# Optimization experiments

Measured on AMD Instinct MI355X. Metric: run time of the kernel, lower is better.

The kernel has to match this reference:

```python
import jax, jax.numpy as jnp
import numpy as np

BS, T, NE, NA, ED = 32, 64, 32, 8, 128
H, A, NH, NACT = 512, 512, 8, 32
HD = A // NH  # 64
SCALE = np.float32(np.sqrt(HD))


def setup_inputs() -> dict:
    key = jax.random.key(0)
    ks = jax.random.split(key, 12)
    inputs = jax.random.normal(ks[0], (BS, T, NE, ED), jnp.float32)
    obs_mask = jax.random.randint(ks[1], (BS, T, NE, NE), 0, 2, jnp.int32)
    scenario_mask = jax.random.randint(ks[2], (BS, T, NE), 0, 2, jnp.int32)
    hidden_state = jnp.zeros((BS * NA, H), jnp.float32)
    g = lambda k, shp: jax.random.normal(k, shp, jnp.float32) * 0.05
    return {
        'inputs': inputs, 'obs_mask': obs_mask, 'scenario_mask': scenario_mask,
        'hidden_state': hidden_state,
        'W1': g(ks[3], (ED, H)), 'b1': jnp.zeros((H,), jnp.float32),
        'Wq': g(ks[4], (H, A)), 'bq': jnp.zeros((A,), jnp.float32),
        'Wk': g(ks[5], (H, A)), 'bk': jnp.zeros((A,), jnp.float32),
        'Wv': g(ks[6], (H, A)), 'bv': jnp.zeros((A,), jnp.float32),
        'Wih': g(ks[7], (3 * H, A)), 'bih': jnp.zeros((3 * H,), jnp.float32),
        'Whh': g(ks[8], (3 * H, H)), 'bhh': jnp.zeros((3 * H,), jnp.float32),
        'Wo': g(ks[9], (H, NACT)), 'bo': jnp.zeros((NACT,), jnp.float32),
    }


def reference(inputs, obs_mask, scenario_mask, hidden_state,
              W1, b1, Wq, bq, Wk, bk, Wv, bv, Wih, bih, Whh, bhh, Wo, bo):
    # fc1: embed every entity  [BS,T,NE,H]
    x = jax.nn.relu(inputs @ W1 + b1)
    q = (x @ Wq + bq).reshape(BS, T, NE, NH, HD)[:, :, :NA]   # agent queries
    k = (x @ Wk + bk).reshape(BS, T, NE, NH, HD)
    v = jax.nn.relu(x @ Wv + bv).reshape(BS, T, NE, NH, HD)
    # scores [BS,T,NH,NA,NE]
    score = jnp.einsum('btqhe,btkhe->bthqk', q, k) / SCALE
    am = obs_mask[:, :, :NA, :].astype(bool)                  # [BS,T,NA,NE]
    score = jnp.where(am[:, :, None], -jnp.inf, score)
    w = jax.nn.softmax(score, axis=-1)
    w = jnp.where(jnp.isnan(w), 0.0, w)                       # fully-masked rows -> 0
    att = jnp.einsum('bthqk,btkhe->btqhe', w, v).reshape(BS, T, NA, A)
    agent_mask = scenario_mask[:, :, :NA].astype(bool)        # [BS,T,NA]
    att = jnp.where(agent_mask[..., None], 0.0, att)
    # per-timestep GRUCell over flattened (BS*NA) rows
    xs = att.transpose(1, 0, 2, 3).reshape(T, BS * NA, A)
    def step(h, xt):
        gi = xt @ Wih.T + bih
        gh = h @ Whh.T + bhh
        ir, iz, inn = jnp.split(gi, 3, axis=-1)
        hr, hz, hn = jnp.split(gh, 3, axis=-1)
        r = jax.nn.sigmoid(ir + hr)
        z = jax.nn.sigmoid(iz + hz)
        n = jnp.tanh(inn + r * hn)
        hn_ = (1.0 - z) * n + z * h
        return hn_, hn_
    _, hs = jax.lax.scan(step, hidden_state, xs)              # [T,BS*NA,H]
    hs = hs.reshape(T, BS, NA, H).transpose(1, 0, 2, 3)       # [BS,T,NA,H]
    qout = hs @ Wo + bo                                       # [BS,T,NA,NACT]
    hs = jnp.where(agent_mask[..., None], 0.0, hs)
    qout = jnp.where(agent_mask[..., None], 0.0, qout)
    return qout, hs
```

## Files before the change

### kernel.cpp

```cpp
#include <hip/hip_runtime.h>
#include <hip/hip_bf16.h>
#include <cstddef>
#include <cstdint>

typedef __hip_bfloat16 bf16;
typedef __attribute__((ext_vector_type(2))) _Float16 half2v;
typedef __attribute__((ext_vector_type(8))) _Float16 half8;
typedef __attribute__((ext_vector_type(8))) short short8;
typedef __attribute__((ext_vector_type(4))) float f32x4;
typedef __attribute__((ext_vector_type(2))) unsigned long long u64x2;

__device__ inline float ldf(const float* p) { return *p; }
__device__ inline float ldf(const bf16* p) { return __bfloat162float(*p); }
__device__ inline void stf(float* p, float v) { *p = v; }
__device__ inline void stf(bf16* p, float v) { *p = __float2bfloat16(v); }
__device__ inline short bfb(float v) { return __builtin_bit_cast(short, __float2bfloat16(v)); }

__device__ inline half8 h8_from(unsigned long long lo, unsigned long long hi) {
    u64x2 t; t.x = lo; t.y = hi;
    return __builtin_bit_cast(half8, t);
}
__device__ inline float fsig(float x) {
    x = fminf(fmaxf(x, -60.f), 60.f);
    return 1.f / (1.f + __expf(-x));
}
__device__ inline float ftanh(float x) {
    x = fminf(fmaxf(x, -15.f), 15.f);
    float e = __expf(2.f * x);
    return 1.f - 2.f / (e + 1.f);
}
__device__ inline void unpack8(uint4 u, float4& lo, float4& hi) {
    uint32_t w0 = u.x, w1 = u.y, w2 = u.z, w3 = u.w;
    lo.x = __builtin_bit_cast(float, (w0 & 0xffffu) << 16);
    lo.y = __builtin_bit_cast(float, w0 & 0xffff0000u);
    lo.z = __builtin_bit_cast(float, (w1 & 0xffffu) << 16);
    lo.w = __builtin_bit_cast(float, w1 & 0xffff0000u);
    hi.x = __builtin_bit_cast(float, (w2 & 0xffffu) << 16);
    hi.y = __builtin_bit_cast(float, w2 & 0xffff0000u);
    hi.z = __builtin_bit_cast(float, (w3 & 0xffffu) << 16);
    hi.w = __builtin_bit_cast(float, w3 & 0xffff0000u);
}


template<int ACT, bool QG, typename TA, typename TC>
__global__ __launch_bounds__(256) void mfma_gemm_k(
    const TA* __restrict__ A, const bf16* __restrict__ Bt,
    const float* __restrict__ bias, TC* __restrict__ C,
    int M, int N, int K)
{
    __shared__ short As[4096];
    __shared__ short Bs[4096];
    const int tid = threadIdx.x;
    const int lane = tid & 63, wid = tid >> 6;
    const int wm = wid >> 1, wn = wid & 1;
    const int bm = blockIdx.y * 128, bn = blockIdx.x * 128;
    const int fr = lane & 15, fq = lane >> 4;

    f32x4 acc[4][4] = {};

    for (int k0 = 0; k0 < K; k0 += 32) {
#if __has_builtin(__builtin_amdgcn_global_load_lds)
        #pragma unroll
        for (int j = 0; j < 2; ++j) {
            int jj = wid * 2 + j;
            int row = jj * 16 + (lane >> 2);
            const short* src = (const short*)Bt + (size_t)(bn + row) * K + k0 + (lane & 3) * 8;
            __builtin_amdgcn_global_load_lds(
                (const __attribute__((address_space(1))) void*)src,
                (__attribute__((address_space(3))) void*)&Bs[jj * 512], 16, 0, 0);
        }
        if constexpr (sizeof(TA) == 2) {
            #pragma unroll
            for (int j = 0; j < 2; ++j) {
                int jj = wid * 2 + j;
                int row = jj * 16 + (lane >> 2);
                int gm = bm + row;
                int ar = QG ? (((gm >> 3) << 5) | (gm & 7)) : gm;
                const short* src = (const short*)A + (size_t)ar * K + k0 + (lane & 3) * 8;
                __builtin_amdgcn_global_load_lds(
                    (const __attribute__((address_space(1))) void*)src,
                    (__attribute__((address_space(3))) void*)&As[jj * 512], 16, 0, 0);
            }
        } else {
            int sr = tid >> 1, sk = (tid & 1) * 16;
            int gm = bm + sr;
            int ar = QG ? (((gm >> 3) << 5) | (gm & 7)) : gm;
            const float* ap = (const float*)A + (size_t)ar * K + k0 + sk;
            float4 f0 = *(const float4*)(ap);
            float4 f1 = *(const float4*)(ap + 4);
            float4 f2 = *(const float4*)(ap + 8);
            float4 f3 = *(const float4*)(ap + 12);
            short tmp[16] = {bfb(f0.x), bfb(f0.y), bfb(f0.z), bfb(f0.w),
                             bfb(f1.x), bfb(f1.y), bfb(f1.z), bfb(f1.w),
                             bfb(f2.x), bfb(f2.y), bfb(f2.z), bfb(f2.w),
                             bfb(f3.x), bfb(f3.y), bfb(f3.z), bfb(f3.w)};
            *(uint4*)&As[sr * 32 + sk]     = *(const uint4*)&tmp[0];
            *(uint4*)&As[sr * 32 + sk + 8] = *(const uint4*)&tmp[8];
        }
#else
        {
            int sr = tid >> 1, sk = (tid & 1) * 16;
            int gm = bm + sr;
            int ar = QG ? (((gm >> 3) << 5) | (gm & 7)) : gm;
            if constexpr (sizeof(TA) == 4) {
                const float* ap = (const float*)A + (size_t)ar * K + k0 + sk;
                short tmp[16];
                #pragma unroll
                for (int j = 0; j < 16; ++j) tmp[j] = bfb(ap[j]);
                *(uint4*)&As[sr * 32 + sk]     = *(const uint4*)&tmp[0];
                *(uint4*)&As[sr * 32 + sk + 8] = *(const uint4*)&tmp[8];
            } else {
                const short* ap = (const short*)A + (size_t)ar * K + k0 + sk;
                *(uint4*)&As[sr * 32 + sk]     = *(const uint4*)(ap);
                *(uint4*)&As[sr * 32 + sk + 8] = *(const uint4*)(ap + 8);
            }
            const short* bp = (const short*)Bt + (size_t)(bn + sr) * K + k0 + sk;
            *(uint4*)&Bs[sr * 32 + sk]     = *(const uint4*)(bp);
            *(uint4*)&Bs[sr * 32 + sk + 8] = *(const uint4*)(bp + 8);
        }
#endif
        __syncthreads();

        short8 af[4], bg[4];
        #pragma unroll
        for (int m = 0; m < 4; ++m)
            af[m] = *(const short8*)&As[(wm * 64 + m * 16 + fr) * 32 + fq * 8];
        #pragma unroll
        for (int n = 0; n < 4; ++n)
            bg[n] = *(const short8*)&Bs[(wn * 64 + n * 16 + fr) * 32 + fq * 8];
        #pragma unroll
        for (int m = 0; m < 4; ++m)
            #pragma unroll
            for (int n = 0; n < 4; ++n)
                acc[m][n] = __builtin_amdgcn_mfma_f32_16x16x32_bf16(
                    af[m], bg[n], acc[m][n], 0, 0, 0);
        __syncthreads();
    }

    #pragma unroll
    for (int m = 0; m < 4; ++m) {
        #pragma unroll
        for (int n = 0; n < 4; ++n) {
            int col = bn + wn * 64 + n * 16 + fr;
            float bv = bias[col];
            #pragma unroll
            for (int r = 0; r < 4; ++r) {
                int row = bm + wm * 64 + m * 16 + fq * 4 + r;
                float v = acc[m][n][r] + bv;
                if (ACT == 1) v = fmaxf(v, 0.f);
                if (ACT == 2 && col >= 512) v = fmaxf(v, 0.f);
                stf(&C[(size_t)row * N + col], v);
            }
        }
    }
}

__global__ __launch_bounds__(256) void prep_all_k(
    const float* __restrict__ W1, const float* __restrict__ Wq,
    const float* __restrict__ Wk, const float* __restrict__ Wv,
    const float* __restrict__ Wo, const float* __restrict__ h0,
    const float* __restrict__ bk, const float* __restrict__ bv,
    bf16* __restrict__ W1t, bf16* __restrict__ Wqt, bf16* __restrict__ Wkvt,
    bf16* __restrict__ Wot, _Float16* __restrict__ ha, float* __restrict__ bkv)
{
    int blk = blockIdx.x;
    int tid = threadIdx.x;
    if (blk < 848) {
        const float* src; bf16* dst; int K, N, ti;
        if (blk < 64)       { src = W1; dst = W1t;  K = 128; N = 512; ti = blk; }
        else if (blk < 320) { src = Wq; dst = Wqt;  K = 512; N = 512; ti = blk - 64; }
        else if (blk < 576) { src = Wk; dst = Wkvt; K = 512; N = 512; ti = blk - 320; }
        else if (blk < 832) { src = Wv; dst = Wkvt + 512 * 512; K = 512; N = 512; ti = blk - 576; }
        else                { src = Wo; dst = Wot;  K = 512; N = 32;  ti = blk - 832; }
        int kt = K >> 5;
        int tk = ti % kt, tn = ti / kt;
        int k0 = tk * 32, n0 = tn * 32;
        __shared__ float tile[32][33];
        int tx = tid & 31, ty = tid >> 5;
        #pragma unroll
        for (int i = 0; i < 4; ++i) {
            int r = ty + i * 8;
            tile[r][tx] = src[(size_t)(k0 + r) * N + n0 + tx];
        }
        __syncthreads();
        #pragma unroll
        for (int i = 0; i < 4; ++i) {
            int r = ty + i * 8;
            if (n0 + r < N)
                dst[(size_t)(n0 + r) * K + k0 + tx] = __float2bfloat16(tile[tx][r]);
        }
        return;
    }
    int idx = (blk - 848) * 256 + tid;
    if (idx < 131072) { ha[idx] = (_Float16)h0[idx]; return; }
    idx -= 131072;
    if (idx < 1024) { bkv[idx] = (idx < 512) ? bk[idx] : bv[idx - 512]; return; }
}

__global__ __launch_bounds__(256) void qout_mfma_k(
    const float* __restrict__ hs, const bf16* __restrict__ Wot,
    const float* __restrict__ bo, const int* __restrict__ smask,
    float* __restrict__ out)
{
    __shared__ short Bs2[32 * 520];
    __shared__ short As2[128 * 32];
    const int tid = threadIdx.x;
    const int lane = tid & 63, wid = tid >> 6;
    const int bm = blockIdx.x * 128;
    const int fr = lane & 15, fq = lane >> 4;

    for (int i = tid; i < 2048; i += 256) {
        int row = i >> 6, col = (i & 63) * 8;
        *(uint4*)&Bs2[row * 520 + col] = *(const uint4*)((const short*)Wot + row * 512 + col);
    }

    f32x4 acc[2][2] = {};
    for (int k0 = 0; k0 < 512; k0 += 32) {
        {
            int sr = tid >> 1, sk = (tid & 1) * 16;
            const float* ap = hs + (size_t)(bm + sr) * 512 + k0 + sk;
            float4 f0 = *(const float4*)(ap);
            float4 f1 = *(const float4*)(ap + 4);
            float4 f2 = *(const float4*)(ap + 8);
            float4 f3 = *(const float4*)(ap + 12);
            short tmp[16] = {bfb(f0.x), bfb(f0.y), bfb(f0.z), bfb(f0.w),
                             bfb(f1.x), bfb(f1.y), bfb(f1.z), bfb(f1.w),
                             bfb(f2.x), bfb(f2.y), bfb(f2.z), bfb(f2.w),
                             bfb(f3.x), bfb(f3.y), bfb(f3.z), bfb(f3.w)};
            *(uint4*)&As2[sr * 32 + sk]     = *(const uint4*)&tmp[0];
            *(uint4*)&As2[sr * 32 + sk + 8] = *(const uint4*)&tmp[8];
        }
        __syncthreads();
        short8 af[2], bg[2];
        #pragma unroll
        for (int m = 0; m < 2; ++m)
            af[m] = *(const short8*)&As2[(wid * 32 + m * 16 + fr) * 32 + fq * 8];
        #pragma unroll
        for (int n = 0; n < 2; ++n)
            bg[n] = *(const short8*)&Bs2[(n * 16 + fr) * 520 + k0 + fq * 8];
        #pragma unroll
        for (int m = 0; m < 2; ++m)
            #pragma unroll
            for (int n = 0; n < 2; ++n)
                acc[m][n] = __builtin_amdgcn_mfma_f32_16x16x32_bf16(
                    af[m], bg[n], acc[m][n], 0, 0, 0);
        __syncthreads();
    }

    #pragma unroll
    for (int m = 0; m < 2; ++m) {
        #pragma unroll
        for (int n = 0; n < 2; ++n) {
            int col = n * 16 + fr;
            float bv = bo[col];
            #pragma unroll
            for (int r = 0; r < 4; ++r) {
                int row = bm + wid * 32 + m * 16 + fq * 4 + r;
                int a_ = row & 7, t_ = (row >> 3) & 63, b_ = row >> 9;
                bool mz = smask[((b_ << 6) + t_) * 32 + a_] != 0;
                out[(size_t)row * 32 + col] = mz ? 0.f : (acc[m][n][r] + bv);
            }
        }
    }
}

#define AST 68
__global__ __launch_bounds__(64) void attn_k(
    const bf16* __restrict__ qb, const bf16* __restrict__ kb, const bf16* __restrict__ vb,
    const int* __restrict__ obs, const int* __restrict__ smask, bf16* __restrict__ xs,
    int kvstride)
{
    __shared__ float qs[8 * AST], ks[32 * AST], vs[32 * AST], wsm[8 * 32];
    int bid = blockIdx.x;
    int h = bid & 7;
    int bt = bid >> 3;
    int t = bt & 63, b = bt >> 6;
    int tid = threadIdx.x;

    {
        int srow = tid >> 3, c0 = (tid & 7) * 8;
        float4 lo, hi;
        uint4 qv = *(const uint4*)&qb[((size_t)bt * 8 + srow) * 512 + h * 64 + c0];
        unpack8(qv, lo, hi);
        *(float4*)&qs[srow * AST + c0] = lo;
        *(float4*)&qs[srow * AST + c0 + 4] = hi;
        #pragma unroll
        for (int i = 0; i < 4; ++i) {
            int row = srow + i * 8;
            uint4 kv4 = *(const uint4*)&kb[((size_t)bt * 32 + row) * kvstride + h * 64 + c0];
            unpack8(kv4, lo, hi);
            *(float4*)&ks[row * AST + c0] = lo;
            *(float4*)&ks[row * AST + c0 + 4] = hi;
            uint4 vv4 = *(const uint4*)&vb[((size_t)bt * 32 + row) * kvstride + h * 64 + c0];
            unpack8(vv4, lo, hi);
            *(float4*)&vs[row * AST + c0] = lo;
            *(float4*)&vs[row * AST + c0 + 4] = hi;
        }
    }
    __syncthreads();

    int ql = tid >> 3, jl = tid & 7;
    float s[4];
    #pragma unroll
    for (int c = 0; c < 4; ++c) {
        int kl = jl + c * 8;
        float acc = 0.f;
        for (int d = 0; d < 64; ++d) acc += qs[ql * AST + d] * ks[kl * AST + d];
        acc *= 0.125f;
        bool m = obs[(((size_t)bt * 32) + ql) * 32 + kl] != 0;
        s[c] = m ? -__builtin_inff() : acc;
    }
    float mx = fmaxf(fmaxf(s[0], s[1]), fmaxf(s[2], s[3]));
    for (int off = 1; off < 8; off <<= 1) mx = fmaxf(mx, __shfl_xor(mx, off));
    float e4[4]; float sum = 0.f;
    bool allmasked = (mx == -__builtin_inff());
    #pragma unroll
    for (int c = 0; c < 4; ++c) {
        e4[c] = (allmasked || s[c] == -__builtin_inff()) ? 0.f : expf(s[c] - mx);
        sum += e4[c];
    }
    for (int off = 1; off < 8; off <<= 1) sum += __shfl_xor(sum, off);
    float inv = (sum > 0.f) ? 1.f / sum : 0.f;
    #pragma unroll
    for (int c = 0; c < 4; ++c) wsm[ql * 32 + jl + c * 8] = e4[c] * inv;
    __syncthreads();

    bool amask = smask[(size_t)bt * 32 + ql] != 0;
    #pragma unroll
    for (int dd = 0; dd < 8; ++dd) {
        int d = jl + dd * 8;
        float acc = 0.f;
        for (int kl = 0; kl < 32; ++kl) acc += wsm[ql * 32 + kl] * vs[kl * AST + d];
        if (amask) acc = 0.f;
        xs[((size_t)(t * 256 + b * 8 + ql)) * 512 + h * 64 + d] = __float2bfloat16(acc);
    }
}

__global__ __launch_bounds__(128, 1) void gru_xcd_k(
    const bf16* __restrict__ xs, const float* __restrict__ Wih,
    const float* __restrict__ bih,
    const float* __restrict__ Whh, const float* __restrict__ bhh,
    const float* __restrict__ h0,
    const int* __restrict__ smask, float* __restrict__ hs_out,
    _Float16* __restrict__ ha, _Float16* __restrict__ hb,
    unsigned char* __restrict__ flags8)
{
    __shared__ _Float16 wh16[48 * 520];
    __shared__ short    wi16[48 * 520];
    const int tid = threadIdx.x;
    const int lane = tid & 63, wid = tid >> 6;
    const int g = blockIdx.x;
    const int grp = g & 7, cu = g >> 3;
    const int r0 = grp * 32;
    const int hc0 = cu * 16;
    const int fr = lane & 15, fq = lane >> 4;
    const int hcol = hc0 + fr;
    const int rw0 = r0 + wid * 16;
    const int row0 = rw0 + fq * 4;

    for (int i = tid; i < 6144; i += 128) {
        int flat = i * 4;
        int r = flat >> 9, c = flat & 511;
        int wr = (r >> 4) * 512 + hc0 + (r & 15);
        float4 v = *(const float4*)(Whh + (size_t)wr * 512 + c);
        half2v p0; p0[0] = (_Float16)v.x; p0[1] = (_Float16)v.y;
        half2v p1; p1[0] = (_Float16)v.z; p1[1] = (_Float16)v.w;
        *(uint32_t*)&wh16[r * 520 + c]     = __builtin_bit_cast(uint32_t, p0);
        *(uint32_t*)&wh16[r * 520 + c + 2] = __builtin_bit_cast(uint32_t, p1);
        float4 u = *(const float4*)(Wih + (size_t)wr * 512 + c);
        uint32_t w0 = (uint32_t)(uint16_t)bfb(u.x) | ((uint32_t)(uint16_t)bfb(u.y) << 16);
        uint32_t w1 = (uint32_t)(uint16_t)bfb(u.z) | ((uint32_t)(uint16_t)bfb(u.w) << 16);
        *(uint32_t*)&wi16[r * 520 + c]     = w0;
        *(uint32_t*)&wi16[r * 520 + c + 2] = w1;
    }

    const float bhr = bhh[hcol], bhz = bhh[512 + hcol], bhn = bhh[1024 + hcol];
    const float bir = bih[hcol], biz = bih[512 + hcol], bin_ = bih[1024 + hcol];

    float hp[4];
    #pragma unroll
    for (int r = 0; r < 4; ++r)
        hp[r] = h0[(size_t)(row0 + r) * 512 + hcol];

    __syncthreads();

    f32x4 gcur[3] = {};
    int mcur[4];
    {
        const short* xp = (const short*)xs + ((size_t)0 * 256 + rw0 + fr) * 512 + fq * 8;
        short8 ax[16];
        #pragma unroll
        for (int ks = 0; ks < 16; ++ks) ax[ks] = *(const short8*)(xp + ks * 32);
        #pragma unroll
        for (int ks = 0; ks < 16; ++ks) {
            const short* bb = &wi16[fr * 520 + ks * 32 + fq * 8];
            short8 b0 = *(const short8*)(bb);
            short8 b1 = *(const short8*)(bb + 16 * 520);
            short8 b2 = *(const short8*)(bb + 32 * 520);
            gcur[0] = __builtin_amdgcn_mfma_f32_16x16x32_bf16(ax[ks], b0, gcur[0], 0, 0, 0);
            gcur[1] = __builtin_amdgcn_mfma_f32_16x16x32_bf16(ax[ks], b1, gcur[1], 0, 0, 0);
            gcur[2] = __builtin_amdgcn_mfma_f32_16x16x32_bf16(ax[ks], b2, gcur[2], 0, 0, 0);
        }
        #pragma unroll
        for (int r = 0; r < 4; ++r) {
            int row = row0 + r;
            mcur[r] = smask[(((row >> 3) << 6) + 0) * 32 + (row & 7)];
        }
    }

    for (int t = 0; t < 64; ++t) {
        const _Float16* hsrc = (t & 1) ? hb : ha;
        _Float16*       hdst = (t & 1) ? ha : hb;

        half8 aA[16];
        {
            const unsigned long long* ap = (const unsigned long long*)
                (hsrc + (size_t)(rw0 + fr) * 512 + fq * 8);
            #pragma unroll
            for (int ks = 0; ks < 16; ++ks) {
                unsigned long long lo = __hip_atomic_load(ap + ks * 8,
                    __ATOMIC_RELAXED, __HIP_MEMORY_SCOPE_AGENT);
                unsigned long long hi = __hip_atomic_load(ap + ks * 8 + 1,
                    __ATOMIC_RELAXED, __HIP_MEMORY_SCOPE_AGENT);
                aA[ks] = h8_from(lo, hi);
            }
        }

        f32x4 acc[3] = {};
        #pragma unroll
        for (int ks = 0; ks < 16; ++ks) {
            const _Float16* bbase = &wh16[fr * 520 + ks * 32 + fq * 8];
            half8 b0 = *(const half8*)(bbase);
            half8 b1 = *(const half8*)(bbase + 16 * 520);
            half8 b2 = *(const half8*)(bbase + 32 * 520);
            acc[0] = __builtin_amdgcn_mfma_f32_16x16x32_f16(aA[ks], b0, acc[0], 0, 0, 0);
            acc[1] = __builtin_amdgcn_mfma_f32_16x16x32_f16(aA[ks], b1, acc[1], 0, 0, 0);
            acc[2] = __builtin_amdgcn_mfma_f32_16x16x32_f16(aA[ks], b2, acc[2], 0, 0, 0);
        }

        float hnv[4];
        #pragma unroll
        for (int r = 0; r < 4; ++r) {
            float rg = fsig(gcur[0][r] + bir + acc[0][r] + bhr);
            float zg = fsig(gcur[1][r] + biz + acc[1][r] + bhz);
            float ng = ftanh(gcur[2][r] + bin_ + rg * (acc[2][r] + bhn));
            float hn = (1.f - zg) * ng + zg * hp[r];
            hp[r] = hn;
            hnv[r] = hn;
            unsigned short hbits = __builtin_bit_cast(unsigned short, (_Float16)hn);
            __hip_atomic_store((unsigned short*)(hdst + (size_t)(row0 + r) * 512 + hcol),
                               hbits, __ATOMIC_RELAXED, __HIP_MEMORY_SCOPE_AGENT);
        }

        if (t != 63) {
            asm volatile("s_waitcnt vmcnt(0)" ::: "memory");
            __builtin_amdgcn_sched_barrier(0);
            if (lane == 0)
                __hip_atomic_store(flags8 + ((size_t)grp * 64 + t) * 64 + cu * 2 + wid,
                                   (unsigned char)1,
                                   __ATOMIC_RELAXED, __HIP_MEMORY_SCOPE_AGENT);
            #pragma unroll
            for (int r = 0; r < 4; ++r) {
                int row = row0 + r;
                int b_ = row >> 3, a_ = row & 7;
                hs_out[((size_t)((b_ << 6) + t) * 8 + a_) * 512 + hcol] =
                    mcur[r] ? 0.f : hnv[r];
            }
            f32x4 gnx[3] = {};
            {
                const short* xp = (const short*)xs +
                    ((size_t)(t + 1) * 256 + rw0 + fr) * 512 + fq * 8;
                short8 ax[16];
                #pragma unroll
                for (int ks = 0; ks < 16; ++ks) ax[ks] = *(const short8*)(xp + ks * 32);
                #pragma unroll
                for (int ks = 0; ks < 16; ++ks) {
                    const short* bb = &wi16[fr * 520 + ks * 32 + fq * 8];
                    short8 b0 = *(const short8*)(bb);
                    short8 b1 = *(const short8*)(bb + 16 * 520);
                    short8 b2 = *(const short8*)(bb + 32 * 520);
                    gnx[0] = __builtin_amdgcn_mfma_f32_16x16x32_bf16(ax[ks], b0, gnx[0], 0, 0, 0);
                    gnx[1] = __builtin_amdgcn_mfma_f32_16x16x32_bf16(ax[ks], b1, gnx[1], 0, 0, 0);
                    gnx[2] = __builtin_amdgcn_mfma_f32_16x16x32_bf16(ax[ks], b2, gnx[2], 0, 0, 0);
                }
            }
            int mnx[4];
            #pragma unroll
            for (int r = 0; r < 4; ++r) {
                int row = row0 + r;
                mnx[r] = smask[(((row >> 3) << 6) + (t + 1)) * 32 + (row & 7)];
            }
            const unsigned char* fp = flags8 + ((size_t)grp * 64 + t) * 64 + lane;
            long it = 0;
            for (;;) {
                unsigned char f = __hip_atomic_load(fp, __ATOMIC_RELAXED,
                                                    __HIP_MEMORY_SCOPE_AGENT);
                if (__all(f != 0) || it > 200000000L) break;
                ++it;
            }
            __builtin_amdgcn_sched_barrier(0);
            gcur[0] = gnx[0]; gcur[1] = gnx[1]; gcur[2] = gnx[2];
            mcur[0] = mnx[0]; mcur[1] = mnx[1]; mcur[2] = mnx[2]; mcur[3] = mnx[3];
        } else {
            #pragma unroll
            for (int r = 0; r < 4; ++r) {
                int row = row0 + r;
                int b_ = row >> 3, a_ = row & 7;
                hs_out[((size_t)((b_ << 6) + t) * 8 + a_) * 512 + hcol] =
                    mcur[r] ? 0.f : hnv[r];
            }
        }
    }
}

extern "C" void kernel_launch(void* const* d_in, const int* in_sizes, int n_in,
                              void* d_out, int out_size, void* d_ws, size_t ws_size,
                              hipStream_t stream)
{
    const float* inputs = (const float*)d_in[0];
    const int*   obs    = (const int*)d_in[1];
    const int*   smask  = (const int*)d_in[2];
    const float* h0     = (const float*)d_in[3];
    const float* W1  = (const float*)d_in[4];  const float* b1  = (const float*)d_in[5];
    const float* Wq  = (const float*)d_in[6];  const float* bq  = (const float*)d_in[7];
    const float* Wk  = (const float*)d_in[8];  const float* bk  = (const float*)d_in[9];
    const float* Wv  = (const float*)d_in[10]; const float* bv  = (const float*)d_in[11];
    const float* Wih = (const float*)d_in[12]; const float* bih = (const float*)d_in[13];
    const float* Whh = (const float*)d_in[14]; const float* bhh = (const float*)d_in[15];
    const float* Wo  = (const float*)d_in[16]; const float* bo  = (const float*)d_in[17];

    char* ws = (char*)d_ws;
    bf16*  x    = (bf16*)(ws + 0);
    bf16*  xs   = (bf16*)(ws + 0);
    bf16*  qb   = (bf16*)(ws + 67108864ull);
    bf16*  kv   = (bf16*)(ws + 83886080ull);
    bf16*  W1t  = (bf16*)(ws + 218103808ull);
    bf16*  Wqt  = (bf16*)(ws + 218234880ull);
    bf16*  Wkvt = (bf16*)(ws + 218759168ull);
    _Float16* ha = (_Float16*)(ws + 219807744ull);
    _Float16* hb = (_Float16*)(ws + 220069888ull);
    unsigned char* flags8 = (unsigned char*)(ws + 220332032ull);
    float* bkv  = (float*)(ws + 220364800ull);
    bf16*  Wot  = (bf16*)(ws + 220368896ull);

    float* out    = (float*)d_out;
    float* hs_out = out + 524288;

    hipMemsetAsync(flags8, 0, 32768, stream);

    prep_all_k<<<dim3(1365), 256, 0, stream>>>(
        W1, Wq, Wk, Wv, Wo, h0, bk, bv, W1t, Wqt, Wkvt, Wot, ha, bkv);
    mfma_gemm_k<1, false, float, bf16><<<dim3(4, 512), 256, 0, stream>>>(
        inputs, W1t, b1, x, 65536, 512, 128);
    mfma_gemm_k<0, true, bf16, bf16><<<dim3(4, 128), 256, 0, stream>>>(
        x, Wqt, bq, qb, 16384, 512, 512);
    mfma_gemm_k<2, false, bf16, bf16><<<dim3(8, 512), 256, 0, stream>>>(
        x, Wkvt, bkv, kv, 65536, 1024, 512);
    attn_k<<<dim3(16384), 64, 0, stream>>>(qb, kv, kv + 512, obs, smask, xs, 1024);
    gru_xcd_k<<<dim3(256), 128, 0, stream>>>(
        xs, Wih, bih, Whh, bhh, h0, smask, hs_out, ha, hb, flags8);
    qout_mfma_k<<<dim3(128), 256, 0, stream>>>(hs_out, Wot, bo, smask, out);
}
```

Baseline: 642.6 us.

## Double-buffer GEMM LDS tiles and widen GRU sync flags with sleeping spin

The MFMA GEMM now keeps two LDS buffers for the A and B tiles. It issues the global-to-LDS loads for the next K-slice before computing on the current one, so load latency can overlap the MFMA work, at the cost of twice the shared memory per block. Separately, the GRU's inter-block step flags change from bytes to 32-bit ints, and the spin-wait loop gains an s_sleep. This is meant to cut memory contention from polling, but it may add wake-up latency on the sequential recurrence's critical path. The workspace offsets and the flag memset size are adjusted to match.

```diff
diff --git a/kernel.cpp b/kernel.cpp
--- a/kernel.cpp
+++ b/kernel.cpp
@@ -48,8 +48,8 @@
     const float* __restrict__ bias, TC* __restrict__ C,
     int M, int N, int K)
 {
-    __shared__ short As[4096];
-    __shared__ short Bs[4096];
+    __shared__ short As[2][4096];
+    __shared__ short Bs[2][4096];
     const int tid = threadIdx.x;
     const int lane = tid & 63, wid = tid >> 6;
     const int wm = wid >> 1, wn = wid & 1;
@@ -58,7 +58,7 @@
 
     f32x4 acc[4][4] = {};
 
-    for (int k0 = 0; k0 < K; k0 += 32) {
+    auto stage = [&](int buf, int k0) {
 #if __has_builtin(__builtin_amdgcn_global_load_lds)
         #pragma unroll
         for (int j = 0; j < 2; ++j) {
@@ -67,7 +67,7 @@
             const short* src = (const short*)Bt + (size_t)(bn + row) * K + k0 + (lane & 3) * 8;
             __builtin_amdgcn_global_load_lds(
                 (const __attribute__((address_space(1))) void*)src,
-                (__attribute__((address_space(3))) void*)&Bs[jj * 512], 16, 0, 0);
+                (__attribute__((address_space(3))) void*)&Bs[buf][jj * 512], 16, 0, 0);
         }
         if constexpr (sizeof(TA) == 2) {
             #pragma unroll
@@ -79,7 +79,7 @@
                 const short* src = (const short*)A + (size_t)ar * K + k0 + (lane & 3) * 8;
                 __builtin_amdgcn_global_load_lds(
                     (const __attribute__((address_space(1))) void*)src,
-                    (__attribute__((address_space(3))) void*)&As[jj * 512], 16, 0, 0);
+                    (__attribute__((address_space(3))) void*)&As[buf][jj * 512], 16, 0, 0);
             }
         } else {
             int sr = tid >> 1, sk = (tid & 1) * 16;
@@ -94,8 +94,8 @@
                              bfb(f1.x), bfb(f1.y), bfb(f1.z), bfb(f1.w),
                              bfb(f2.x), bfb(f2.y), bfb(f2.z), bfb(f2.w),
                              bfb(f3.x), bfb(f3.y), bfb(f3.z), bfb(f3.w)};
-            *(uint4*)&As[sr * 32 + sk]     = *(const uint4*)&tmp[0];
-            *(uint4*)&As[sr * 32 + sk + 8] = *(const uint4*)&tmp[8];
+            *(uint4*)&As[buf][sr * 32 + sk]     = *(const uint4*)&tmp[0];
+            *(uint4*)&As[buf][sr * 32 + sk + 8] = *(const uint4*)&tmp[8];
         }
 #else
         {
@@ -107,27 +107,35 @@
                 short tmp[16];
                 #pragma unroll
                 for (int j = 0; j < 16; ++j) tmp[j] = bfb(ap[j]);
-                *(uint4*)&As[sr * 32 + sk]     = *(const uint4*)&tmp[0];
-                *(uint4*)&As[sr * 32 + sk + 8] = *(const uint4*)&tmp[8];
+                *(uint4*)&As[buf][sr * 32 + sk]     = *(const uint4*)&tmp[0];
+                *(uint4*)&As[buf][sr * 32 + sk + 8] = *(const uint4*)&tmp[8];
             } else {
                 const short* ap = (const short*)A + (size_t)ar * K + k0 + sk;
-                *(uint4*)&As[sr * 32 + sk]     = *(const uint4*)(ap);
-                *(uint4*)&As[sr * 32 + sk + 8] = *(const uint4*)(ap + 8);
+                *(uint4*)&As[buf][sr * 32 + sk]     = *(const uint4*)(ap);
+                *(uint4*)&As[buf][sr * 32 + sk + 8] = *(const uint4*)(ap + 8);
             }
             const short* bp = (const short*)Bt + (size_t)(bn + sr) * K + k0 + sk;
-            *(uint4*)&Bs[sr * 32 + sk]     = *(const uint4*)(bp);
-            *(uint4*)&Bs[sr * 32 + sk + 8] = *(const uint4*)(bp + 8);
+            *(uint4*)&Bs[buf][sr * 32 + sk]     = *(const uint4*)(bp);
+            *(uint4*)&Bs[buf][sr * 32 + sk + 8] = *(const uint4*)(bp + 8);
         }
 #endif
-        __syncthreads();
+    };
+
+    const int nt = K >> 5;
+    stage(0, 0);
+    __syncthreads();
+
+    for (int t = 0; t < nt; ++t) {
+        int cur = t & 1;
+        if (t + 1 < nt) stage(cur ^ 1, (t + 1) * 32);
 
         short8 af[4], bg[4];
         #pragma unroll
         for (int m = 0; m < 4; ++m)
-            af[m] = *(const short8*)&As[(wm * 64 + m * 16 + fr) * 32 + fq * 8];
+            af[m] = *(const short8*)&As[cur][(wm * 64 + m * 16 + fr) * 32 + fq * 8];
         #pragma unroll
         for (int n = 0; n < 4; ++n)
-            bg[n] = *(const short8*)&Bs[(wn * 64 + n * 16 + fr) * 32 + fq * 8];
+            bg[n] = *(const short8*)&Bs[cur][(wn * 64 + n * 16 + fr) * 32 + fq * 8];
         #pragma unroll
         for (int m = 0; m < 4; ++m)
             #pragma unroll
@@ -342,8 +350,7 @@
     const float* __restrict__ Whh, const float* __restrict__ bhh,
     const float* __restrict__ h0,
     const int* __restrict__ smask, float* __restrict__ hs_out,
-    _Float16* __restrict__ ha, _Float16* __restrict__ hb,
-    unsigned char* __restrict__ flags8)
+    _Float16* __restrict__ ha, _Float16* __restrict__ hb, int* __restrict__ flags)
 {
     __shared__ _Float16 wh16[48 * 520];
     __shared__ short    wi16[48 * 520];
@@ -456,8 +463,7 @@
             asm volatile("s_waitcnt vmcnt(0)" ::: "memory");
             __builtin_amdgcn_sched_barrier(0);
             if (lane == 0)
-                __hip_atomic_store(flags8 + ((size_t)grp * 64 + t) * 64 + cu * 2 + wid,
-                                   (unsigned char)1,
+                __hip_atomic_store(flags + ((size_t)grp * 64 + t) * 64 + cu * 2 + wid, 1,
                                    __ATOMIC_RELAXED, __HIP_MEMORY_SCOPE_AGENT);
             #pragma unroll
             for (int r = 0; r < 4; ++r) {
@@ -490,12 +496,12 @@
                 int row = row0 + r;
                 mnx[r] = smask[(((row >> 3) << 6) + (t + 1)) * 32 + (row & 7)];
             }
-            const unsigned char* fp = flags8 + ((size_t)grp * 64 + t) * 64 + lane;
+            const int* fp = flags + ((size_t)grp * 64 + t) * 64 + lane;
             long it = 0;
             for (;;) {
-                unsigned char f = __hip_atomic_load(fp, __ATOMIC_RELAXED,
-                                                    __HIP_MEMORY_SCOPE_AGENT);
-                if (__all(f != 0) || it > 200000000L) break;
+                int f = __hip_atomic_load(fp, __ATOMIC_RELAXED, __HIP_MEMORY_SCOPE_AGENT);
+                if (__all(f != 0) || it > 100000000L) break;
+                __builtin_amdgcn_s_sleep(1);
                 ++it;
             }
             __builtin_amdgcn_sched_barrier(0);
@@ -539,14 +545,14 @@
     bf16*  Wkvt = (bf16*)(ws + 218759168ull);
     _Float16* ha = (_Float16*)(ws + 219807744ull);
     _Float16* hb = (_Float16*)(ws + 220069888ull);
-    unsigned char* flags8 = (unsigned char*)(ws + 220332032ull);
-    float* bkv  = (float*)(ws + 220364800ull);
-    bf16*  Wot  = (bf16*)(ws + 220368896ull);
+    int*   flags = (int*)(ws + 220332032ull);
+    float* bkv  = (float*)(ws + 220463104ull);
+    bf16*  Wot  = (bf16*)(ws + 220467200ull);
 
     float* out    = (float*)d_out;
     float* hs_out = out + 524288;
 
-    hipMemsetAsync(flags8, 0, 32768, stream);
+    hipMemsetAsync(flags, 0, 131072, stream);
 
     prep_all_k<<<dim3(1365), 256, 0, stream>>>(
         W1, Wq, Wk, Wv, Wo, h0, bk, bv, W1t, Wqt, Wkvt, Wot, ha, bkv);
@@ -558,6 +564,6 @@
         x, Wkvt, bkv, kv, 65536, 1024, 512);
     attn_k<<<dim3(16384), 64, 0, stream>>>(qb, kv, kv + 512, obs, smask, xs, 1024);
     gru_xcd_k<<<dim3(256), 128, 0, stream>>>(
-        xs, Wih, bih, Whh, bhh, h0, smask, hs_out, ha, hb, flags8);
+        xs, Wih, bih, Whh, bhh, h0, smask, hs_out, ha, hb, flags);
     qout_mfma_k<<<dim3(128), 256, 0, stream>>>(hs_out, Wot, bo, smask, out);
 }
```

New measurement: 600.7 us. 1.07x faster.
